# Kernel tuning notes

Hardware: AMD Instinct MI355X
Metric: run time of the kernel (lower is better)

## Reference

```python
import jax, jax.numpy as jnp
import numpy as np

NUM_HEADS = 8
NUM_GROUPS = 8
NUM_ITERATIONS = 3
DT = 0.1
EPS = 1e-5


def group_norm(x, scale, bias):
    # x: [B, C, H, W], GroupNorm(8, C)
    B, C, H, W = x.shape
    xg = x.reshape(B, NUM_GROUPS, C // NUM_GROUPS, H, W)
    mean = xg.mean(axis=(2, 3, 4), keepdims=True)
    var = xg.var(axis=(2, 3, 4), keepdims=True)
    xg = (xg - mean) * jax.lax.rsqrt(var + EPS)
    x = xg.reshape(B, C, H, W)
    return x * scale[None, :, None, None] + bias[None, :, None, None]


def setup_inputs() -> dict:
    key = jax.random.key(0)
    ks = jax.random.split(key, 4)
    B, C, H, W = 8, 512, 32, 32
    x = jax.random.normal(ks[0], (B, C, H, W), dtype=jnp.float32)
    qkv_w = jax.random.normal(ks[1], (3 * C, C), dtype=jnp.float32) * (1.0 / np.sqrt(C))
    proj_w = jax.random.normal(ks[2], (C, C), dtype=jnp.float32) * (1.0 / np.sqrt(C))
    inl_w = jax.random.normal(ks[3], (C, C), dtype=jnp.float32) * (1.0 / np.sqrt(C))
    return {
        "x": x,
        "gn_scale": jnp.ones((C,), jnp.float32),
        "gn_bias": jnp.zeros((C,), jnp.float32),
        "qkv_w": qkv_w,
        "qkv_b": jnp.zeros((3 * C,), jnp.float32),
        "proj_w": proj_w,
        "proj_b": jnp.zeros((C,), jnp.float32),
        "inl_w": inl_w,
        "inl_b": jnp.zeros((C,), jnp.float32),
    }


def reference(x, gn_scale, gn_bias, qkv_w, qkv_b, proj_w, proj_b, inl_w, inl_b):
    B, C, H, W = x.shape
    nh = NUM_HEADS
    hd = C // nh
    S = H * W

    h = group_norm(x, gn_scale, gn_bias)

    # 1x1 conv == channel matmul
    qkv = jnp.einsum('oc,bchw->bohw', qkv_w, h) + qkv_b[None, :, None, None]
    q, k, v = jnp.split(qkv, 3, axis=1)  # each [B, C, H, W]

    def to_heads(t):  # [B, C, H, W] -> [B, nh, S, hd]
        return t.reshape(B, nh, hd, S).transpose(0, 1, 3, 2)

    q, k, v = to_heads(q), to_heads(k), to_heads(v)

    scale = hd ** (-0.5)
    attn = jax.nn.softmax(jnp.einsum('bnsd,bntd->bnst', q, k) * scale, axis=-1)
    h = jnp.einsum('bnst,bntd->bnsd', attn, v)  # [B, nh, S, hd]

    # back to [B, S, C] for INL refinement
    h_flat = h.transpose(0, 1, 3, 2).reshape(B, C, S).transpose(0, 2, 1)

    # SimpleINLDynamics: iterative Euler refinement x <- x + dt * tanh(W x + b)
    def step(hf, _):
        hf = hf + DT * jnp.tanh(jnp.einsum('bsc,oc->bso', hf, inl_w) + inl_b)
        return hf, None
    h_flat, _ = jax.lax.scan(step, h_flat, None, length=NUM_ITERATIONS)

    h = h_flat.transpose(0, 2, 1).reshape(B, C, H, W)
    h = jnp.einsum('oc,bchw->bohw', proj_w, h) + proj_b[None, :, None, None]
    return x + h
```

## Files before the change

kernel.cpp:

```cpp
#include <hip/hip_runtime.h>
#include <math.h>

#define B_ 8
#define C_ 512
#define S_ 1024
#define HD 64
#define NHEADS 8
#define NGROUPS 8
#define DT_STEP 0.1f
#define EPS_GN 1e-5f
#define LOG2E 1.4426950408889634f

typedef __attribute__((ext_vector_type(8))) short bf16x8;
typedef __attribute__((ext_vector_type(4))) float f32x4;
typedef __attribute__((ext_vector_type(8))) unsigned short ushort8;
typedef __attribute__((ext_vector_type(4))) unsigned short ushort4_t;

static __device__ __forceinline__ unsigned short f2bf(float f) {
  unsigned int u = __builtin_bit_cast(unsigned int, f);
  u += 0x7fff + ((u >> 16) & 1);
  return (unsigned short)(u >> 16);
}

static __device__ __forceinline__ unsigned short f2bf_fast(float f) {
  unsigned int u = __builtin_bit_cast(unsigned int, f);
  return (unsigned short)((u + 0x8000u) >> 16);
}

static __device__ __forceinline__ float bf2f(unsigned short u) {
  unsigned int t = ((unsigned int)u) << 16;
  return __builtin_bit_cast(float, t);
}

static __device__ __forceinline__ float exp2_raw(float x) {
  return __builtin_amdgcn_exp2f(x);
}

static __device__ __forceinline__ float fast_tanh(float x) {
  float xc = fminf(fmaxf(x, -15.f), 15.f);
  float e = exp2_raw(xc * (2.0f * LOG2E));
  return (e - 1.f) / (e + 1.f);
}

static __device__ __forceinline__ void load16_lds(const void* g, void* l) {
  __builtin_amdgcn_global_load_lds((const __attribute__((address_space(1))) void*)g,
                                   (__attribute__((address_space(3))) void*)l, 16, 0, 0);
}

__global__ __launch_bounds__(256) void prep_kernel(
    const float* __restrict__ a, const float* __restrict__ b, const float* __restrict__ c,
    unsigned short* __restrict__ A, unsigned short* __restrict__ B, unsigned short* __restrict__ C,
    const float* __restrict__ x, float* __restrict__ gpart) {
  int bid = blockIdx.x;
  int tid = threadIdx.x;
  if (bid < 640) {
    const float* src; unsigned short* dst; int off;
    if (bid < 384) { src = a; dst = A; off = bid * 2048; }
    else if (bid < 512) { src = b; dst = B; off = (bid - 384) * 2048; }
    else { src = c; dst = C; off = (bid - 512) * 2048; }
    int i = off + tid * 8;
    f32x4 v0 = *(const f32x4*)(src + i);
    f32x4 v1 = *(const f32x4*)(src + i + 4);
    ushort8 o;
    o[0] = f2bf(v0[0]); o[1] = f2bf(v0[1]); o[2] = f2bf(v0[2]); o[3] = f2bf(v0[3]);
    o[4] = f2bf(v1[0]); o[5] = f2bf(v1[1]); o[6] = f2bf(v1[2]); o[7] = f2bf(v1[3]);
    *(ushort8*)(dst + i) = o;
    return;
  }
  int sbid = bid - 640;
  int bg = sbid >> 3, chunk = sbid & 7;
  const float* xp = x + (size_t)bg * 65536 + (size_t)chunk * 8192;
  float sum = 0.f, sq = 0.f;
  #pragma unroll
  for (int i = 0; i < 8; ++i) {
    f32x4 v = *(const f32x4*)(xp + i * 1024 + tid * 4);
    sum += v[0] + v[1] + v[2] + v[3];
    sq += v[0]*v[0] + v[1]*v[1] + v[2]*v[2] + v[3]*v[3];
  }
  #pragma unroll
  for (int off = 32; off >= 1; off >>= 1) {
    sum += __shfl_xor(sum, off, 64);
    sq  += __shfl_xor(sq, off, 64);
  }
  __shared__ float s1[4], s2[4];
  int wave = tid >> 6, lane = tid & 63;
  if (lane == 0) { s1[wave] = sum; s2[wave] = sq; }
  __syncthreads();
  if (tid == 0) {
    float S = s1[0] + s1[1] + s1[2] + s1[3];
    float Q = s2[0] + s2[1] + s2[2] + s2[3];
    gpart[bg * 16 + chunk * 2] = S;
    gpart[bg * 16 + chunk * 2 + 1] = Q;
  }
}

__global__ __launch_bounds__(256) void gn_apply_t(
    const float* __restrict__ x, const float* __restrict__ gpart,
    const float* __restrict__ scale, const float* __restrict__ bias,
    unsigned short* __restrict__ h_t) {
  int bid = blockIdx.x;
  int bg = bid >> 4, st = bid & 15;
  int b = bg >> 3, g = bg & 7;
  float S = 0.f, Q = 0.f;
  #pragma unroll
  for (int i = 0; i < 8; ++i) {
    S += gpart[bg * 16 + i * 2];
    Q += gpart[bg * 16 + i * 2 + 1];
  }
  float mean = S / 65536.f;
  float var = Q / 65536.f - mean * mean;
  float inv = rsqrtf(var + EPS_GN);

  int tid = threadIdx.x;
  int sl = tid >> 2;
  int cq = (tid & 3) * 16;
  float sA[16], sB[16];
  #pragma unroll
  for (int u = 0; u < 16; ++u) {
    float scv = scale[g * 64 + cq + u];
    sA[u] = inv * scv;
    sB[u] = bias[g * 64 + cq + u] - mean * inv * scv;
  }

  const float* xp = x + ((size_t)b * C_ + (size_t)g * 64) * S_;
  __shared__ float tile[64][65];
  #pragma unroll
  for (int it = 0; it < 16; ++it) {
    int lin = it * 256 + tid;
    int c = lin >> 6, s = lin & 63;
    tile[c][s] = xp[(size_t)c * S_ + st * 64 + s];
  }
  __syncthreads();
  unsigned short vals[16];
  #pragma unroll
  for (int u = 0; u < 16; ++u)
    vals[u] = f2bf_fast(tile[cq + u][sl] * sA[u] + sB[u]);
  unsigned short* dst = h_t + ((size_t)b * S_ + st * 64 + sl) * C_ + g * 64 + cq;
  ushort8 lo, hi;
  #pragma unroll
  for (int u = 0; u < 8; ++u) { lo[u] = vals[u]; hi[u] = vals[u + 8]; }
  *(ushort8*)dst = lo;
  *(ushort8*)(dst + 8) = hi;
}

template<int MB, int NB, int WMG, int WNG>
__device__ __forceinline__ void gemm_nt_core(
    const unsigned short* __restrict__ Ab,
    const unsigned short* __restrict__ Bb,
    unsigned short* ldsA, unsigned short* ldsB,
    f32x4* acc) {
  constexpr int TI = (MB / WMG) / 16;
  constexpr int TJ = (NB / WNG) / 16;
  constexpr int NQA = MB * 4 / 256;
  constexpr int NQB = NB * 4 / 256;
  const int K = 512;
  const int tid = threadIdx.x;
  const int w = tid >> 6, lane = tid & 63, quad = lane >> 4, l15 = lane & 15;
  const int wm = (WNG == 1) ? w : ((WMG == 1) ? 0 : (w >> 1));
  const int wn = (WNG == 1) ? 0 : ((WMG == 1) ? w : (w & 1));

  for (int k0 = 0; k0 < K; k0 += 32) {
    __syncthreads();
    #pragma unroll
    for (int q = 0; q < NQA; ++q) {
      int c = q * 256 + tid;
      load16_lds(Ab + (size_t)(c >> 2) * K + k0 + (c & 3) * 8, ldsA + c * 8);
    }
    #pragma unroll
    for (int q = 0; q < NQB; ++q) {
      int c = q * 256 + tid;
      load16_lds(Bb + (size_t)(c >> 2) * K + k0 + (c & 3) * 8, ldsB + c * 8);
    }
    __syncthreads();
    bf16x8 af[TI], bfr[TJ];
    #pragma unroll
    for (int i = 0; i < TI; ++i)
      af[i] = *(const bf16x8*)(ldsA + (wm * (MB / WMG) + i * 16 + l15) * 32 + quad * 8);
    #pragma unroll
    for (int j = 0; j < TJ; ++j)
      bfr[j] = *(const bf16x8*)(ldsB + (wn * (NB / WNG) + j * 16 + l15) * 32 + quad * 8);
    #pragma unroll
    for (int i = 0; i < TI; ++i)
      #pragma unroll
      for (int j = 0; j < TJ; ++j)
        acc[i * TJ + j] = __builtin_amdgcn_mfma_f32_16x16x32_bf16(af[i], bfr[j], acc[i * TJ + j], 0, 0, 0);
  }
}

__global__ __launch_bounds__(256) void gemm_qkv_mfma(
    const unsigned short* __restrict__ Wbf, const unsigned short* __restrict__ h_t,
    const float* __restrict__ bias,
    unsigned short* __restrict__ Qt, unsigned short* __restrict__ Kt,
    unsigned short* __restrict__ Vt) {
  __shared__ __align__(16) unsigned short ldsA[128 * 32];
  __shared__ __align__(16) unsigned short ldsB[128 * 32];
  int b = blockIdx.z;
  int bm = blockIdx.y * 128, bn = blockIdx.x * 128;
  f32x4 acc[16];
  #pragma unroll
  for (int t = 0; t < 16; ++t) acc[t] = (f32x4){0.f, 0.f, 0.f, 0.f};
  gemm_nt_core<128, 128, 2, 2>(Wbf + (size_t)bm * 512,
                               h_t + ((size_t)b * S_ + bn) * 512, ldsA, ldsB, acc);
  int tid = threadIdx.x, w = tid >> 6, lane = tid & 63, quad = lane >> 4, l15 = lane & 15;
  int wm = w >> 1, wn = w & 1;
  int tensor = bm >> 9;
  float qscale = (tensor == 0) ? 0.125f * LOG2E : 1.0f;
  #pragma unroll
  for (int i = 0; i < 4; ++i) {
    #pragma unroll
    for (int j = 0; j < 4; ++j) {
      int m0 = bm + wm * 64 + i * 16 + quad * 4;
      int ng = bn + wn * 64 + j * 16 + l15;
      f32x4 v = acc[i * 4 + j];
      if (tensor < 2) {
        int head = (m0 >> 6) & 7, d0 = m0 & 63;
        ushort4_t pk;
        #pragma unroll
        for (int r = 0; r < 4; ++r) pk[r] = f2bf((v[r] + bias[m0 + r]) * qscale);
        unsigned short* dst = (tensor ? Kt : Qt) +
            (((size_t)(b * 8 + head) * S_ + ng) * 64 + d0);
        *(ushort4_t*)dst = pk;
      } else {
        #pragma unroll
        for (int r = 0; r < 4; ++r)
          Vt[(size_t)b * (C_ * S_) + (size_t)(m0 - 1024 + r) * S_ + ng] = f2bf(v[r] + bias[m0 + r]);
      }
    }
  }
}

__global__ __launch_bounds__(256) void attn_mfma(
    const unsigned short* __restrict__ Qt,
    const unsigned short* __restrict__ Kt,
    const unsigned short* __restrict__ Vt,
    unsigned short* __restrict__ hflat_bf) {
  int tid = threadIdx.x, wave = tid >> 6, lane = tid & 63;
  int quad = lane >> 4, l15 = lane & 15;
  int bid = blockIdx.x;
  int bn = bid & 63, sblk = bid >> 6, b = bn >> 3, n = bn & 7;
  int s0w = sblk * 64 + wave * 16;

  __shared__ unsigned short k_lds[64][72];
  __shared__ unsigned short v_lds[64][72];
  __shared__ unsigned short p_lds[4][16][72];

  const unsigned short* Qb = Qt + (((size_t)(b * 8 + n)) * S_ + s0w + l15) * 64;
  const unsigned short* Kb = Kt + ((size_t)(b * 8 + n)) * S_ * 64;
  const unsigned short* Vb = Vt + ((size_t)b * C_ + n * 64) * S_;

  bf16x8 qa0 = *(const bf16x8*)(Qb + quad * 8);
  bf16x8 qa1 = *(const bf16x8*)(Qb + 32 + quad * 8);

  bf16x8 ones;
  #pragma unroll
  for (int j = 0; j < 8; ++j) ones[j] = (short)0x3F80;

  f32x4 o_acc[4];
  f32x4 l_acc = {0.f, 0.f, 0.f, 0.f};
  #pragma unroll
  for (int dc = 0; dc < 4; ++dc) o_acc[dc] = (f32x4){0.f, 0.f, 0.f, 0.f};

  int row0 = tid >> 3, c80 = (tid & 7) * 8;
  int row1 = (tid + 256) >> 3, c81 = c80;

  ushort8 kreg[2], vreg[2];
  kreg[0] = *(const ushort8*)(Kb + (size_t)row0 * 64 + c80);
  kreg[1] = *(const ushort8*)(Kb + (size_t)row1 * 64 + c81);
  vreg[0] = *(const ushort8*)(Vb + (size_t)row0 * S_ + c80);
  vreg[1] = *(const ushort8*)(Vb + (size_t)row1 * S_ + c81);

  for (int t0 = 0; t0 < S_; t0 += 64) {
    __syncthreads();
    *(ushort8*)&k_lds[row0][c80] = kreg[0];
    *(ushort8*)&k_lds[row1][c81] = kreg[1];
    *(ushort8*)&v_lds[row0][c80] = vreg[0];
    *(ushort8*)&v_lds[row1][c81] = vreg[1];
    __syncthreads();
    if (t0 + 64 < S_) {
      int t1 = t0 + 64;
      kreg[0] = *(const ushort8*)(Kb + (size_t)(t1 + row0) * 64 + c80);
      kreg[1] = *(const ushort8*)(Kb + (size_t)(t1 + row1) * 64 + c81);
      vreg[0] = *(const ushort8*)(Vb + (size_t)row0 * S_ + t1 + c80);
      vreg[1] = *(const ushort8*)(Vb + (size_t)row1 * S_ + t1 + c81);
    }

    f32x4 sc[4];
    #pragma unroll
    for (int tc = 0; tc < 4; ++tc) {
      bf16x8 kb0 = *(const bf16x8*)&k_lds[tc * 16 + l15][quad * 8];
      bf16x8 kb1 = *(const bf16x8*)&k_lds[tc * 16 + l15][32 + quad * 8];
      f32x4 c = {0.f, 0.f, 0.f, 0.f};
      c = __builtin_amdgcn_mfma_f32_16x16x32_bf16(qa0, kb0, c, 0, 0, 0);
      sc[tc] = __builtin_amdgcn_mfma_f32_16x16x32_bf16(qa1, kb1, c, 0, 0, 0);
    }

    #pragma unroll
    for (int tc = 0; tc < 4; ++tc)
      #pragma unroll
      for (int r = 0; r < 4; ++r)
        p_lds[wave][quad * 4 + r][tc * 16 + l15] = f2bf_fast(exp2_raw(sc[tc][r]));

    bf16x8 pa0 = *(const bf16x8*)&p_lds[wave][l15][quad * 8];
    bf16x8 pa1 = *(const bf16x8*)&p_lds[wave][l15][32 + quad * 8];
    l_acc = __builtin_amdgcn_mfma_f32_16x16x32_bf16(pa0, ones, l_acc, 0, 0, 0);
    l_acc = __builtin_amdgcn_mfma_f32_16x16x32_bf16(pa1, ones, l_acc, 0, 0, 0);
    #pragma unroll
    for (int dc = 0; dc < 4; ++dc) {
      bf16x8 vb0 = *(const bf16x8*)&v_lds[dc * 16 + l15][quad * 8];
      bf16x8 vb1 = *(const bf16x8*)&v_lds[dc * 16 + l15][32 + quad * 8];
      o_acc[dc] = __builtin_amdgcn_mfma_f32_16x16x32_bf16(pa0, vb0, o_acc[dc], 0, 0, 0);
      o_acc[dc] = __builtin_amdgcn_mfma_f32_16x16x32_bf16(pa1, vb1, o_acc[dc], 0, 0, 0);
    }
  }

  float inv_l[4];
  #pragma unroll
  for (int r = 0; r < 4; ++r) inv_l[r] = 1.f / l_acc[r];
  #pragma unroll
  for (int dc = 0; dc < 4; ++dc) {
    #pragma unroll
    for (int r = 0; r < 4; ++r) {
      int s = s0w + quad * 4 + r;
      size_t idx = ((size_t)b * S_ + s) * C_ + n * 64 + dc * 16 + l15;
      hflat_bf[idx] = f2bf_fast(o_acc[dc][r] * inv_l[r]);
    }
  }
}

__global__ __launch_bounds__(256) void inl_step_mfma(
    const unsigned short* __restrict__ hbf_in, const unsigned short* __restrict__ Wbf,
    const float* __restrict__ bias, unsigned short* __restrict__ hbf_out) {
  __shared__ __align__(16) unsigned short ldsA[64 * 32];
  __shared__ __align__(16) unsigned short ldsB[64 * 32];
  int bm = blockIdx.y * 64, bn = blockIdx.x * 64;
  f32x4 acc[4];
  #pragma unroll
  for (int t = 0; t < 4; ++t) acc[t] = (f32x4){0.f, 0.f, 0.f, 0.f};
  gemm_nt_core<64, 64, 2, 2>(hbf_in + (size_t)bm * 512,
                             Wbf + (size_t)bn * 512, ldsA, ldsB, acc);
  int tid = threadIdx.x, w = tid >> 6, lane = tid & 63, quad = lane >> 4, l15 = lane & 15;
  int wm = w >> 1, wn = w & 1;
  #pragma unroll
  for (int i = 0; i < 2; ++i) {
    #pragma unroll
    for (int j = 0; j < 2; ++j) {
      int m0 = bm + wm * 32 + i * 16 + quad * 4;
      int o = bn + wn * 32 + j * 16 + l15;
      float bv = bias[o];
      f32x4 v = acc[i * 2 + j];
      #pragma unroll
      for (int r = 0; r < 4; ++r) {
        size_t idx = (size_t)(m0 + r) * 512 + o;
        float hin = bf2f(hbf_in[idx]);
        hbf_out[idx] = f2bf_fast(hin + DT_STEP * fast_tanh(v[r] + bv));
      }
    }
  }
}

__global__ __launch_bounds__(256) void gemm_proj_mfma(
    const unsigned short* __restrict__ Wbf, const unsigned short* __restrict__ hbf,
    const float* __restrict__ pb, const float* __restrict__ x,
    float* __restrict__ Out) {
  __shared__ __align__(16) unsigned short ldsA[64 * 32];
  __shared__ __align__(16) unsigned short ldsB[64 * 32];
  int bm = blockIdx.y * 64, bn = blockIdx.x * 64;
  f32x4 acc[4];
  #pragma unroll
  for (int t = 0; t < 4; ++t) acc[t] = (f32x4){0.f, 0.f, 0.f, 0.f};
  gemm_nt_core<64, 64, 2, 2>(Wbf + (size_t)bm * 512,
                             hbf + (size_t)bn * 512, ldsA, ldsB, acc);
  int tid = threadIdx.x, w = tid >> 6, lane = tid & 63, quad = lane >> 4, l15 = lane & 15;
  int wm = w >> 1, wn = w & 1;
  #pragma unroll
  for (int i = 0; i < 2; ++i) {
    #pragma unroll
    for (int j = 0; j < 2; ++j) {
      int o0 = bm + wm * 32 + i * 16 + quad * 4;
      int ng = bn + wn * 32 + j * 16 + l15;
      int b = ng >> 10, s = ng & 1023;
      f32x4 v = acc[i * 2 + j];
      #pragma unroll
      for (int r = 0; r < 4; ++r) {
        size_t idx = ((size_t)b * C_ + o0 + r) * S_ + s;
        Out[idx] = x[idx] + pb[o0 + r] + v[r];
      }
    }
  }
}

extern "C" void kernel_launch(void* const* d_in, const int* in_sizes, int n_in,
                              void* d_out, int out_size, void* d_ws, size_t ws_size,
                              hipStream_t stream) {
  const float* x        = (const float*)d_in[0];
  const float* gn_scale = (const float*)d_in[1];
  const float* gn_bias  = (const float*)d_in[2];
  const float* qkv_w    = (const float*)d_in[3];
  const float* qkv_b    = (const float*)d_in[4];
  const float* proj_w   = (const float*)d_in[5];
  const float* proj_b   = (const float*)d_in[6];
  const float* inl_w    = (const float*)d_in[7];
  const float* inl_b    = (const float*)d_in[8];
  float* out = (float*)d_out;
  float* ws = (float*)d_ws;

  unsigned short* Qt  = (unsigned short*)(ws + 8388608);
  unsigned short* Kt  = (unsigned short*)(ws + 10485760);
  unsigned short* Vt  = (unsigned short*)(ws + 12582912);
  unsigned short* h_t = (unsigned short*)(ws + 14680064);
  unsigned short* Bbf = h_t;
  unsigned short* Abf = (unsigned short*)(ws + 16777216);
  float* gpart = ws + 18874368;
  unsigned short* qkvw_bf  = (unsigned short*)(ws + 18878464);
  unsigned short* inlw_bf  = qkvw_bf + 786432;
  unsigned short* projw_bf = inlw_bf + 262144;

  prep_kernel<<<1152, 256, 0, stream>>>(qkv_w, inl_w, proj_w, qkvw_bf, inlw_bf, projw_bf, x, gpart);
  gn_apply_t<<<1024, 256, 0, stream>>>(x, gpart, gn_scale, gn_bias, h_t);
  gemm_qkv_mfma<<<dim3(8, 12, 8), 256, 0, stream>>>(qkvw_bf, h_t, qkv_b, Qt, Kt, Vt);
  attn_mfma<<<1024, 256, 0, stream>>>(Qt, Kt, Vt, Abf);
  inl_step_mfma<<<dim3(8, 128), 256, 0, stream>>>(Abf, inlw_bf, inl_b, Bbf);
  inl_step_mfma<<<dim3(8, 128), 256, 0, stream>>>(Bbf, inlw_bf, inl_b, Abf);
  inl_step_mfma<<<dim3(8, 128), 256, 0, stream>>>(Abf, inlw_bf, inl_b, Bbf);
  gemm_proj_mfma<<<dim3(128, 8), 256, 0, stream>>>(projw_bf, Bbf, proj_b, x, out);
}
```

Measured before the change: 216.0 us.

## Process two query tiles per wave in attention to reuse K/V LDS tiles

```diff
diff --git a/kernel.cpp b/kernel.cpp
--- a/kernel.cpp
+++ b/kernel.cpp
@@ -238,27 +238,35 @@
   int quad = lane >> 4, l15 = lane & 15;
   int bid = blockIdx.x;
   int bn = bid & 63, sblk = bid >> 6, b = bn >> 3, n = bn & 7;
-  int s0w = sblk * 64 + wave * 16;
+  int s0w = sblk * 128 + wave * 32;
 
   __shared__ unsigned short k_lds[64][72];
   __shared__ unsigned short v_lds[64][72];
-  __shared__ unsigned short p_lds[4][16][72];
-
-  const unsigned short* Qb = Qt + (((size_t)(b * 8 + n)) * S_ + s0w + l15) * 64;
+  __shared__ unsigned short p_lds[4][2][16][72];
+
   const unsigned short* Kb = Kt + ((size_t)(b * 8 + n)) * S_ * 64;
   const unsigned short* Vb = Vt + ((size_t)b * C_ + n * 64) * S_;
 
-  bf16x8 qa0 = *(const bf16x8*)(Qb + quad * 8);
-  bf16x8 qa1 = *(const bf16x8*)(Qb + 32 + quad * 8);
+  bf16x8 qa[2][2];
+  #pragma unroll
+  for (int g = 0; g < 2; ++g) {
+    const unsigned short* Qb = Qt + (((size_t)(b * 8 + n)) * S_ + s0w + g * 16 + l15) * 64;
+    qa[g][0] = *(const bf16x8*)(Qb + quad * 8);
+    qa[g][1] = *(const bf16x8*)(Qb + 32 + quad * 8);
+  }
 
   bf16x8 ones;
   #pragma unroll
   for (int j = 0; j < 8; ++j) ones[j] = (short)0x3F80;
 
-  f32x4 o_acc[4];
-  f32x4 l_acc = {0.f, 0.f, 0.f, 0.f};
-  #pragma unroll
-  for (int dc = 0; dc < 4; ++dc) o_acc[dc] = (f32x4){0.f, 0.f, 0.f, 0.f};
+  f32x4 o_acc[2][4];
+  f32x4 l_acc[2];
+  #pragma unroll
+  for (int g = 0; g < 2; ++g) {
+    l_acc[g] = (f32x4){0.f, 0.f, 0.f, 0.f};
+    #pragma unroll
+    for (int dc = 0; dc < 4; ++dc) o_acc[g][dc] = (f32x4){0.f, 0.f, 0.f, 0.f};
+  }
 
   int row0 = tid >> 3, c80 = (tid & 7) * 8;
   int row1 = (tid + 256) >> 3, c81 = c80;
@@ -284,45 +292,62 @@
       vreg[1] = *(const ushort8*)(Vb + (size_t)row1 * S_ + t1 + c81);
     }
 
-    f32x4 sc[4];
+    f32x4 sc[2][4];
     #pragma unroll
     for (int tc = 0; tc < 4; ++tc) {
       bf16x8 kb0 = *(const bf16x8*)&k_lds[tc * 16 + l15][quad * 8];
       bf16x8 kb1 = *(const bf16x8*)&k_lds[tc * 16 + l15][32 + quad * 8];
-      f32x4 c = {0.f, 0.f, 0.f, 0.f};
-      c = __builtin_amdgcn_mfma_f32_16x16x32_bf16(qa0, kb0, c, 0, 0, 0);
-      sc[tc] = __builtin_amdgcn_mfma_f32_16x16x32_bf16(qa1, kb1, c, 0, 0, 0);
-    }
-
-    #pragma unroll
-    for (int tc = 0; tc < 4; ++tc)
-      #pragma unroll
-      for (int r = 0; r < 4; ++r)
-        p_lds[wave][quad * 4 + r][tc * 16 + l15] = f2bf_fast(exp2_raw(sc[tc][r]));
-
-    bf16x8 pa0 = *(const bf16x8*)&p_lds[wave][l15][quad * 8];
-    bf16x8 pa1 = *(const bf16x8*)&p_lds[wave][l15][32 + quad * 8];
-    l_acc = __builtin_amdgcn_mfma_f32_16x16x32_bf16(pa0, ones, l_acc, 0, 0, 0);
-    l_acc = __builtin_amdgcn_mfma_f32_16x16x32_bf16(pa1, ones, l_acc, 0, 0, 0);
+      #pragma unroll
+      for (int g = 0; g < 2; ++g) {
+        f32x4 c = {0.f, 0.f, 0.f, 0.f};
+        c = __builtin_amdgcn_mfma_f32_16x16x32_bf16(kb0, qa[g][0], c, 0, 0, 0);
+        sc[g][tc] = __builtin_amdgcn_mfma_f32_16x16x32_bf16(kb1, qa[g][1], c, 0, 0, 0);
+      }
+    }
+
+    #pragma unroll
+    for (int g = 0; g < 2; ++g)
+      #pragma unroll
+      for (int tc = 0; tc < 4; ++tc) {
+        ushort4_t p4;
+        #pragma unroll
+        for (int r = 0; r < 4; ++r) p4[r] = f2bf_fast(exp2_raw(sc[g][tc][r]));
+        *(ushort4_t*)&p_lds[wave][g][l15][tc * 16 + quad * 4] = p4;
+      }
+
+    bf16x8 pa[2][2];
+    #pragma unroll
+    for (int g = 0; g < 2; ++g) {
+      pa[g][0] = *(const bf16x8*)&p_lds[wave][g][l15][quad * 8];
+      pa[g][1] = *(const bf16x8*)&p_lds[wave][g][l15][32 + quad * 8];
+      l_acc[g] = __builtin_amdgcn_mfma_f32_16x16x32_bf16(pa[g][0], ones, l_acc[g], 0, 0, 0);
+      l_acc[g] = __builtin_amdgcn_mfma_f32_16x16x32_bf16(pa[g][1], ones, l_acc[g], 0, 0, 0);
+    }
     #pragma unroll
     for (int dc = 0; dc < 4; ++dc) {
       bf16x8 vb0 = *(const bf16x8*)&v_lds[dc * 16 + l15][quad * 8];
       bf16x8 vb1 = *(const bf16x8*)&v_lds[dc * 16 + l15][32 + quad * 8];
-      o_acc[dc] = __builtin_amdgcn_mfma_f32_16x16x32_bf16(pa0, vb0, o_acc[dc], 0, 0, 0);
-      o_acc[dc] = __builtin_amdgcn_mfma_f32_16x16x32_bf16(pa1, vb1, o_acc[dc], 0, 0, 0);
-    }
-  }
-
-  float inv_l[4];
-  #pragma unroll
-  for (int r = 0; r < 4; ++r) inv_l[r] = 1.f / l_acc[r];
-  #pragma unroll
-  for (int dc = 0; dc < 4; ++dc) {
-    #pragma unroll
-    for (int r = 0; r < 4; ++r) {
-      int s = s0w + quad * 4 + r;
-      size_t idx = ((size_t)b * S_ + s) * C_ + n * 64 + dc * 16 + l15;
-      hflat_bf[idx] = f2bf_fast(o_acc[dc][r] * inv_l[r]);
+      #pragma unroll
+      for (int g = 0; g < 2; ++g) {
+        o_acc[g][dc] = __builtin_amdgcn_mfma_f32_16x16x32_bf16(pa[g][0], vb0, o_acc[g][dc], 0, 0, 0);
+        o_acc[g][dc] = __builtin_amdgcn_mfma_f32_16x16x32_bf16(pa[g][1], vb1, o_acc[g][dc], 0, 0, 0);
+      }
+    }
+  }
+
+  #pragma unroll
+  for (int g = 0; g < 2; ++g) {
+    float inv_l[4];
+    #pragma unroll
+    for (int r = 0; r < 4; ++r) inv_l[r] = 1.f / l_acc[g][r];
+    #pragma unroll
+    for (int dc = 0; dc < 4; ++dc) {
+      #pragma unroll
+      for (int r = 0; r < 4; ++r) {
+        int s = s0w + g * 16 + quad * 4 + r;
+        size_t idx = ((size_t)b * S_ + s) * C_ + n * 64 + dc * 16 + l15;
+        hflat_bf[idx] = f2bf_fast(o_acc[g][dc][r] * inv_l[r]);
+      }
     }
   }
 }
@@ -418,7 +443,7 @@
   prep_kernel<<<1152, 256, 0, stream>>>(qkv_w, inl_w, proj_w, qkvw_bf, inlw_bf, projw_bf, x, gpart);
   gn_apply_t<<<1024, 256, 0, stream>>>(x, gpart, gn_scale, gn_bias, h_t);
   gemm_qkv_mfma<<<dim3(8, 12, 8), 256, 0, stream>>>(qkvw_bf, h_t, qkv_b, Qt, Kt, Vt);
-  attn_mfma<<<1024, 256, 0, stream>>>(Qt, Kt, Vt, Abf);
+  attn_mfma<<<512, 256, 0, stream>>>(Qt, Kt, Vt, Abf);
   inl_step_mfma<<<dim3(8, 128), 256, 0, stream>>>(Abf, inlw_bf, inl_b, Bbf);
   inl_step_mfma<<<dim3(8, 128), 256, 0, stream>>>(Bbf, inlw_bf, inl_b, Abf);
   inl_step_mfma<<<dim3(8, 128), 256, 0, stream>>>(Abf, inlw_bf, inl_b, Bbf);
```

New measurement: 208.9 us. -3.3%, faster.
